# Performance work log

Measured on AMD Instinct MI355X. Metric: run time of the kernel, lower is better.

## Reference

```python
import jax, jax.numpy as jnp
from jax import lax
import numpy as np

B, CIN, H, W = 32, 256, 56, 56
BOTTLE, GROWTH = 128, 32
EPS = 1e-5
QMAX = 127.0  # 8-bit symmetric


def _fq(x, scale, qmax=QMAX):
    # fake-quantize with straight-through estimator
    q = jnp.clip(jnp.round(x / scale), -qmax - 1.0, qmax) * scale
    return x + lax.stop_gradient(q - x)


def fake_quant_act(x):
    # per-tensor symmetric 8-bit activation quantization (QuantAct)
    scale = lax.stop_gradient(jnp.max(jnp.abs(x)) / QMAX + 1e-8)
    return _fq(x, scale), scale


def quant_weight_pc(w):
    # per-output-channel symmetric 8-bit weight quantization, w: [O,I,kh,kw]
    scale = lax.stop_gradient(jnp.max(jnp.abs(w), axis=(1, 2, 3)) / QMAX + 1e-8)
    return _fq(w, scale[:, None, None, None]), scale


def conv2d(x, w, pad):
    return lax.conv_general_dilated(
        x, w, window_strides=(1, 1), padding=[(pad, pad), (pad, pad)],
        dimension_numbers=("NCHW", "OIHW", "NCHW"))


def setup_inputs() -> dict:
    key = jax.random.key(0)
    ks = jax.random.split(key, 12)
    return {
        "batch": jax.random.normal(ks[0], (B, CIN, H, W), jnp.float32),
        "input_scaling_factor": jnp.float32(0.05),
        "bn1_gamma": jax.random.uniform(ks[1], (CIN,), jnp.float32, 0.5, 1.5),
        "bn1_beta": jax.random.normal(ks[2], (CIN,), jnp.float32) * 0.1,
        "bn1_mean": jax.random.normal(ks[3], (CIN,), jnp.float32) * 0.1,
        "bn1_var": jax.random.uniform(ks[4], (CIN,), jnp.float32, 0.5, 1.5),
        "conv1_w": jax.random.normal(ks[5], (BOTTLE, CIN, 1, 1), jnp.float32) * 0.05,
        "bn2_gamma": jax.random.uniform(ks[6], (BOTTLE,), jnp.float32, 0.5, 1.5),
        "bn2_beta": jax.random.normal(ks[7], (BOTTLE,), jnp.float32) * 0.1,
        "bn2_mean": jax.random.normal(ks[8], (BOTTLE,), jnp.float32) * 0.1,
        "bn2_var": jax.random.uniform(ks[9], (BOTTLE,), jnp.float32, 0.5, 1.5),
        "conv2_w": jax.random.normal(ks[10], (GROWTH, BOTTLE, 3, 3), jnp.float32) * 0.05,
    }


def reference(batch, input_scaling_factor, bn1_gamma, bn1_beta, bn1_mean,
              bn1_var, conv1_w, bn2_gamma, bn2_beta, bn2_mean, bn2_var,
              conv2_w):
    s_in = input_scaling_factor
    # ---- QuantBn1: BN with fake-quantized folded weight/bias ----
    w1 = bn1_gamma * lax.rsqrt(bn1_var + EPS)            # [CIN]
    b1 = bn1_beta - bn1_mean * w1                        # [CIN]
    s_bn = lax.stop_gradient(jnp.max(jnp.abs(w1)) / QMAX + 1e-8)
    w1q = _fq(w1, s_bn)
    b1q = _fq(b1, s_in * s_bn, qmax=2.0 ** 31)           # bias quantized at s_in*s_w
    x = batch * w1q[None, :, None, None] + b1q[None, :, None, None]
    x = jax.nn.relu(x)                                   # act1
    x, s_a1 = fake_quant_act(x)                          # quant_act1
    # ---- QuantBnConv2d: fold bn2 into conv1 (1x1), per-channel weight quant ----
    t = bn2_gamma * lax.rsqrt(bn2_var + EPS)             # [BOTTLE]
    wf = conv1_w * t[:, None, None, None]
    bf = bn2_beta - bn2_mean * t
    wfq, s_w1 = quant_weight_pc(wf)                      # s_w1: [BOTTLE]
    bfq = _fq(bf, s_a1 * s_w1, qmax=2.0 ** 31)
    x = conv2d(x, wfq, pad=0) + bfq[None, :, None, None]
    x = jax.nn.relu(x)                                   # act2
    x, s_a2 = fake_quant_act(x)                          # quant_act2
    # ---- QuantConv2d: 3x3 growth conv, per-channel weight quant ----
    w2q, s_w2 = quant_weight_pc(conv2_w)
    x = conv2d(x, w2q, pad=1)                            # [B, GROWTH, H, W]
    # ---- concat + output requant ----
    cat = jnp.concatenate([batch, x], axis=1)            # [B, CIN+GROWTH, H, W]
    out, s_out = fake_quant_act(cat)                     # quant_act_output
    return out, s_out
```

## Files before the change

### kernel.cpp

```cpp
#include <hip/hip_runtime.h>

typedef __attribute__((ext_vector_type(8))) short bf16x8;
typedef __attribute__((ext_vector_type(4))) float f32x4;

constexpr int B_   = 32;
constexpr int CIN  = 256;
constexpr int HW   = 56 * 56;
constexpr int BOT  = 128;
constexpr int GRW  = 32;
constexpr int COUT = CIN + GRW;
constexpr int NBATCH = B_ * CIN * HW;
constexpr int NX2    = B_ * BOT * HW;
constexpr int NOUT   = B_ * COUT * HW;

constexpr int NSLOT = 32;
constexpr int SSTR  = 32;
constexpr int OFF_SLOT = 16;
constexpr int OFF_W1Q  = OFF_SLOT + 4 * NSLOT * SSTR;
constexpr int OFF_B1Q  = OFF_W1Q + 256;
constexpr int OFF_BFQ  = OFF_B1Q + 256;
constexpr int OFF_SC1  = OFF_BFQ + 128;
constexpr int OFF_SC2  = OFF_SC1 + 128;
constexpr int OFF_WQ1B = OFF_SC2 + 32;
constexpr int OFF_W2B  = OFF_WQ1B + 16384;
constexpr int OFF_END  = OFF_W2B + 18432;
constexpr size_t X1Q_BYTE = (size_t)OFF_END * 4;
constexpr size_t X2_BYTE  = X1Q_BYTE + (size_t)NBATCH;
constexpr size_t X2Q_BYTE = X1Q_BYTE;
constexpr size_t X3_BYTE  = X2_BYTE + (size_t)NX2 * 4;

__device__ __forceinline__ void slotAtomicMax(float* ws, int a, int s, float v) {
    atomicMax((unsigned*)ws + OFF_SLOT + a * NSLOT * SSTR + s * SSTR, __float_as_uint(v));
}
__device__ __forceinline__ float slotMax(const float* ws, int a) {
    float m = 0.0f;
    #pragma unroll
    for (int s = 0; s < NSLOT; s++)
        m = fmaxf(m, ws[OFF_SLOT + a * NSLOT * SSTR + s * SSTR]);
    return m;
}

__device__ __forceinline__ float blockReduceMax256(float v) {
    #pragma unroll
    for (int o = 32; o > 0; o >>= 1) v = fmaxf(v, __shfl_down(v, o, 64));
    __shared__ float sm[4];
    if ((threadIdx.x & 63) == 0) sm[threadIdx.x >> 6] = v;
    __syncthreads();
    return fmaxf(fmaxf(sm[0], sm[1]), fmaxf(sm[2], sm[3]));
}
__device__ __forceinline__ float waveReduceMax(float v) {
    #pragma unroll
    for (int o = 32; o > 0; o >>= 1) v = fmaxf(v, __shfl_down(v, o, 64));
    return v;
}
__device__ __forceinline__ float clamp8(float r)   { return fminf(fmaxf(r, -128.0f), 127.0f); }
__device__ __forceinline__ float clampBig(float r) { return fminf(fmaxf(r, -2147483648.0f), 2147483648.0f); }
__device__ __forceinline__ unsigned short bf16u(float f) { return (unsigned short)(__float_as_uint(f) >> 16); }

__device__ __forceinline__ bf16x8 b8_to_bf16(uint2 p) {
    bf16x8 r;
    #pragma unroll
    for (int j = 0; j < 4; j++) r[j]     = (short)bf16u((float)((p.x >> (j * 8)) & 255u));
    #pragma unroll
    for (int j = 0; j < 4; j++) r[4 + j] = (short)bf16u((float)((p.y >> (j * 8)) & 255u));
    return r;
}

__global__ void prep1_kernel(const float* __restrict__ g1, const float* __restrict__ b1p,
                             const float* __restrict__ m1, const float* __restrict__ v1,
                             const float* __restrict__ s_in_p, float* __restrict__ ws) {
    int c = threadIdx.x;
    unsigned* scal = (unsigned*)ws;
    for (int s = c; s < OFF_W1Q; s += 256) scal[s] = 0u;
    float s_in = *s_in_p;
    float r = 1.0f / sqrtf(v1[c] + 1e-5f);
    float w1 = __fmul_rn(g1[c], r);
    float b1 = __fsub_rn(b1p[c], __fmul_rn(m1[c], w1));
    float mx = blockReduceMax256(fabsf(w1));
    float s_bn = mx / 127.0f + 1e-8f;
    ws[OFF_W1Q + c] = __fmul_rn(clamp8(rintf(w1 / s_bn)), s_bn);
    float sb = __fmul_rn(s_in, s_bn);
    ws[OFF_B1Q + c] = __fmul_rn(clampBig(rintf(b1 / sb)), sb);
}

__global__ __launch_bounds__(256) void max1_kernel(const float4* __restrict__ batch4,
                                                   float* __restrict__ ws) {
    const float* w1q = ws + OFF_W1Q;
    const float* b1q = ws + OFF_B1Q;
    int n4 = NBATCH / 4;
    float mx1 = 0.0f, mxb = 0.0f;
    for (int i = blockIdx.x * blockDim.x + threadIdx.x; i < n4; i += gridDim.x * blockDim.x) {
        int c = (i / 784) & 255;
        float w = w1q[c], b = b1q[c];
        float4 v = batch4[i];
        float x0 = fmaxf(__fadd_rn(__fmul_rn(v.x, w), b), 0.0f);
        float x1 = fmaxf(__fadd_rn(__fmul_rn(v.y, w), b), 0.0f);
        float x2 = fmaxf(__fadd_rn(__fmul_rn(v.z, w), b), 0.0f);
        float x3 = fmaxf(__fadd_rn(__fmul_rn(v.w, w), b), 0.0f);
        mx1 = fmaxf(mx1, fmaxf(fmaxf(x0, x1), fmaxf(x2, x3)));
        mxb = fmaxf(mxb, fmaxf(fmaxf(fabsf(v.x), fabsf(v.y)), fmaxf(fabsf(v.z), fabsf(v.w))));
    }
    mx1 = blockReduceMax256(mx1);
    __syncthreads();
    mxb = blockReduceMax256(mxb);
    if (threadIdx.x == 0) {
        int s = blockIdx.x & (NSLOT - 1);
        slotAtomicMax(ws, 0, s, mx1);
        slotAtomicMax(ws, 1, s, mxb);
    }
}

__global__ __launch_bounds__(256) void quant1_kernel(const float4* __restrict__ batch4,
                                                     float* __restrict__ ws) {
    __shared__ unsigned ldsq[256 * 16];
    const float* w1q = ws + OFF_W1Q;
    const float* b1q = ws + OFF_B1Q;
    float s_a1 = slotMax(ws, 0) / 127.0f + 1e-8f;
    int b = blockIdx.x / 49, hw0 = (blockIdx.x % 49) * 64;
    int t = threadIdx.x;
    int f = t & 15, cb = t >> 4;
    #pragma unroll
    for (int j = 0; j < 16; j++) {
        int c = cb + j * 16;
        float w = w1q[c], bb = b1q[c];
        float4 v = batch4[(b * 256 + c) * 784 + (hw0 >> 2) + f];
        unsigned q0 = (unsigned)(int)clamp8(rintf(fmaxf(__fadd_rn(__fmul_rn(v.x, w), bb), 0.0f) / s_a1));
        unsigned q1 = (unsigned)(int)clamp8(rintf(fmaxf(__fadd_rn(__fmul_rn(v.y, w), bb), 0.0f) / s_a1));
        unsigned q2 = (unsigned)(int)clamp8(rintf(fmaxf(__fadd_rn(__fmul_rn(v.z, w), bb), 0.0f) / s_a1));
        unsigned q3 = (unsigned)(int)clamp8(rintf(fmaxf(__fadd_rn(__fmul_rn(v.w, w), bb), 0.0f) / s_a1));
        ldsq[c * 16 + f] = q0 | (q1 << 8) | (q2 << 16) | (q3 << 24);
    }
    __syncthreads();
    const unsigned char* l8 = (const unsigned char*)ldsq;
    uint4* outv = (uint4*)((char*)ws + X1Q_BYTE);
    int hwl = t >> 2, cq = (t & 3) * 16;
    #pragma unroll
    for (int k = 0; k < 4; k++) {
        int c0 = cq + k * 64;
        unsigned u[4] = {0u, 0u, 0u, 0u};
        #pragma unroll
        for (int i = 0; i < 16; i++) {
            unsigned by = l8[(c0 + i) * 64 + hwl];
            u[i >> 2] |= by << ((i & 3) * 8);
        }
        uint4 val; val.x = u[0]; val.y = u[1]; val.z = u[2]; val.w = u[3];
        outv[(((size_t)b * 3136 + hw0 + hwl) * 256 + c0) >> 4] = val;
    }
}

__global__ void prep2_kernel(const float* __restrict__ c1w,
                             const float* __restrict__ g2, const float* __restrict__ b2,
                             const float* __restrict__ m2, const float* __restrict__ v2,
                             const float* __restrict__ c2w, float* __restrict__ ws) {
    int bi = blockIdx.x;
    int t = threadIdx.x;
    unsigned short* wq1b = (unsigned short*)(ws + OFF_WQ1B);
    unsigned short* w2b  = (unsigned short*)(ws + OFF_W2B);
    if (bi < BOT) {
        int o = bi;
        float tt = __fmul_rn(g2[o], 1.0f / sqrtf(v2[o] + 1e-5f));
        float wf = __fmul_rn(c1w[o * CIN + t], tt);
        float mx = blockReduceMax256(fabsf(wf));
        float s_w1 = mx / 127.0f + 1e-8f;
        float m = clamp8(rintf(wf / s_w1));
        wq1b[o * CIN + t] = bf16u(m);
        if (t == 0) {
            float s_a1 = slotMax(ws, 0) / 127.0f + 1e-8f;
            ws[OFF_SC1 + o] = __fmul_rn(s_a1, s_w1);
            float bf = __fsub_rn(b2[o], __fmul_rn(m2[o], tt));
            float sb = __fmul_rn(s_a1, s_w1);
            ws[OFF_BFQ + o] = __fmul_rn(clampBig(rintf(bf / sb)), sb);
        }
    } else {
        int g = bi - BOT;
        float mx = 0.0f;
        for (int s = t; s < BOT * 9; s += 256) mx = fmaxf(mx, fabsf(c2w[g * BOT * 9 + s]));
        mx = blockReduceMax256(mx);
        float s_w2 = mx / 127.0f + 1e-8f;
        for (int s = t; s < BOT * 9; s += 256) {
            int c = s / 9, tap = s - c * 9;
            float m = clamp8(rintf(c2w[g * BOT * 9 + s] / s_w2));
            w2b[(tap * GRW + g) * BOT + c] = bf16u(m);
        }
        if (t == 0) ws[OFF_SC2 + g] = s_w2;
    }
}

__global__ __launch_bounds__(256) void conv1_kernel(float* __restrict__ ws) {
    __shared__ unsigned short lA[64 * 136];
    __shared__ unsigned short lW[128 * 136];
    __shared__ float wred[4];
    const unsigned char* x1q = (const unsigned char*)((char*)ws + X1Q_BYTE);
    const unsigned short* wq1b = (const unsigned short*)(ws + OFF_WQ1B);
    const float* sc1 = ws + OFF_SC1;
    const float* bfq = ws + OFF_BFQ;
    float* x2 = (float*)((char*)ws + X2_BYTE);
    int b = blockIdx.x / 49, hw0 = (blockIdx.x % 49) * 64;
    int t = threadIdx.x, lane = t & 63, wv = t >> 6;
    int quad = lane >> 4, l16 = lane & 15;
    int mhalf = wv & 1, nhalf = wv >> 1;
    f32x4 acc[2][4];
    #pragma unroll
    for (int i = 0; i < 2; i++)
        #pragma unroll
        for (int j = 0; j < 4; j++) acc[i][j] = (f32x4){0.f, 0.f, 0.f, 0.f};

    for (int kc = 0; kc < 256; kc += 128) {
        __syncthreads();
        {
            int cb = t & 7, hwi = t >> 3;
            #pragma unroll
            for (int r = 0; r < 2; r++) {
                int hw = hwi + r * 32;
                uint4 p = *(const uint4*)(x1q + ((size_t)b * 3136 + hw0 + hw) * 256 + kc + cb * 16);
                unsigned wd[4] = {p.x, p.y, p.z, p.w};
                bf16x8 t0, t1;
                #pragma unroll
                for (int j = 0; j < 8; j++)
                    t0[j] = (short)bf16u((float)((wd[j >> 2] >> ((j & 3) * 8)) & 255u));
                #pragma unroll
                for (int j = 0; j < 8; j++)
                    t1[j] = (short)bf16u((float)((wd[2 + (j >> 2)] >> ((j & 3) * 8)) & 255u));
                *(bf16x8*)&lA[hw * 136 + cb * 16] = t0;
                *(bf16x8*)&lA[hw * 136 + cb * 16 + 8] = t1;
            }
        }
        {
            int cb = t & 7, oi = t >> 3;
            #pragma unroll
            for (int r = 0; r < 4; r++) {
                int o = oi + r * 32;
                uint4 p0 = *(const uint4*)(wq1b + o * 256 + kc + cb * 16);
                uint4 p1 = *(const uint4*)(wq1b + o * 256 + kc + cb * 16 + 8);
                *(uint4*)&lW[o * 136 + cb * 16] = p0;
                *(uint4*)&lW[o * 136 + cb * 16 + 8] = p1;
            }
        }
        __syncthreads();
        #pragma unroll
        for (int ks = 0; ks < 4; ks++) {
            bf16x8 a0 = *(const bf16x8*)&lA[(mhalf * 32 + l16) * 136 + ks * 32 + quad * 8];
            bf16x8 a1 = *(const bf16x8*)&lA[(mhalf * 32 + 16 + l16) * 136 + ks * 32 + quad * 8];
            #pragma unroll
            for (int nt = 0; nt < 4; nt++) {
                bf16x8 bfr = *(const bf16x8*)&lW[(nhalf * 64 + nt * 16 + l16) * 136 + ks * 32 + quad * 8];
                acc[0][nt] = __builtin_amdgcn_mfma_f32_16x16x32_bf16(a0, bfr, acc[0][nt], 0, 0, 0);
                acc[1][nt] = __builtin_amdgcn_mfma_f32_16x16x32_bf16(a1, bfr, acc[1][nt], 0, 0, 0);
            }
        }
    }
    float mx = 0.0f;
    #pragma unroll
    for (int nt = 0; nt < 4; nt++) {
        int o = nhalf * 64 + nt * 16 + l16;
        float s = sc1[o], bb = bfq[o];
        #pragma unroll
        for (int mt = 0; mt < 2; mt++) {
            int hw = hw0 + mhalf * 32 + mt * 16 + quad * 4;
            float4 v;
            v.x = fmaxf(__fadd_rn(__fmul_rn(acc[mt][nt][0], s), bb), 0.0f);
            v.y = fmaxf(__fadd_rn(__fmul_rn(acc[mt][nt][1], s), bb), 0.0f);
            v.z = fmaxf(__fadd_rn(__fmul_rn(acc[mt][nt][2], s), bb), 0.0f);
            v.w = fmaxf(__fadd_rn(__fmul_rn(acc[mt][nt][3], s), bb), 0.0f);
            mx = fmaxf(mx, fmaxf(fmaxf(v.x, v.y), fmaxf(v.z, v.w)));
            *(float4*)&x2[(size_t)(b * BOT + o) * HW + hw] = v;
        }
    }
    mx = waveReduceMax(mx);
    if (lane == 0) wred[wv] = mx;
    __syncthreads();
    if (t == 0) {
        float m = fmaxf(fmaxf(wred[0], wred[1]), fmaxf(wred[2], wred[3]));
        slotAtomicMax(ws, 2, blockIdx.x & (NSLOT - 1), m);
    }
}

__global__ __launch_bounds__(256) void quant2_kernel(float* __restrict__ ws) {
    __shared__ unsigned ldsq[128 * 16];
    unsigned char* x2q = (unsigned char*)((char*)ws + X2Q_BYTE);
    int b = blockIdx.x / 58, hp = blockIdx.x % 58;
    int t = threadIdx.x;
    uint4* dst = (uint4*)(x2q + ((size_t)(b * 58 + hp) << 13));
    if (hp == 0 || hp == 57) {
        uint4 z; z.x = z.y = z.z = z.w = 0u;
        dst[t] = z; dst[t + 256] = z;
        return;
    }
    int h = hp - 1;
    float s_a2 = slotMax(ws, 2) / 127.0f + 1e-8f;
    float rinv = 1.0f / s_a2;
    const float4* x24 = (const float4*)((char*)ws + X2_BYTE);
    int f = t & 15, cb = t >> 4;
    #pragma unroll
    for (int j = 0; j < 8; j++) {
        int c = cb + j * 16;
        unsigned pk = 0u;
        if (f < 14) {
            float4 v = x24[((size_t)b * 128 + c) * 784 + h * 14 + f];
            unsigned q0 = (unsigned)(int)clamp8(rintf(v.x * rinv)) & 255u;
            unsigned q1 = (unsigned)(int)clamp8(rintf(v.y * rinv)) & 255u;
            unsigned q2 = (unsigned)(int)clamp8(rintf(v.z * rinv)) & 255u;
            unsigned q3 = (unsigned)(int)clamp8(rintf(v.w * rinv)) & 255u;
            pk = q0 | (q1 << 8) | (q2 << 16) | (q3 << 24);
        }
        ldsq[c * 16 + f] = pk;
    }
    __syncthreads();
    const unsigned char* l8 = (const unsigned char*)ldsq;
    #pragma unroll
    for (int k = 0; k < 2; k++) {
        int idx = t + k * 256;
        int wp = idx & 63, cblk = idx >> 6;
        int c0 = cblk * 16;
        unsigned u[4] = {0u, 0u, 0u, 0u};
        if (wp >= 1 && wp <= 56) {
            #pragma unroll
            for (int i = 0; i < 16; i++) {
                unsigned by = l8[(c0 + i) * 64 + (wp - 1)];
                u[i >> 2] |= by << ((i & 3) * 8);
            }
        }
        uint4 val; val.x = u[0]; val.y = u[1]; val.z = u[2]; val.w = u[3];
        dst[wp * 8 + cblk] = val;
    }
}

__global__ __launch_bounds__(256) void conv2_kernel(float* __restrict__ ws) {
    __shared__ unsigned short wt[9 * 32 * 40];
    __shared__ float wred[4];
    const unsigned char* x2q = (const unsigned char*)((char*)ws + X2Q_BYTE);
    const unsigned short* w2b = (const unsigned short*)(ws + OFF_W2B);
    const float* sc2 = ws + OFF_SC2;
    float* x3 = (float*)((char*)ws + X3_BYTE);
    int b = blockIdx.x / 28, hg = blockIdx.x % 28;
    int t = threadIdx.x, lane = t & 63, wv = t >> 6;
    int quad = lane >> 4, l16 = lane & 15;
    int h = hg * 2 + (wv >> 1);
    int wq = wv & 1;
    int w0 = wq * 24;
    float s_a2 = slotMax(ws, 2) / 127.0f + 1e-8f;

    const unsigned char* rowp[2][3];
    #pragma unroll
    for (int mt = 0; mt < 2; mt++) {
        int w = w0 + mt * 16 + l16;
        #pragma unroll
        for (int dh = 0; dh < 3; dh++)
            rowp[mt][dh] = x2q + (((size_t)(b * 58 + h + dh) << 6) + w) * 128 + quad * 8;
    }
    f32x4 acc[2][2];
    #pragma unroll
    for (int i = 0; i < 2; i++) { acc[i][0] = (f32x4){0.f,0.f,0.f,0.f}; acc[i][1] = (f32x4){0.f,0.f,0.f,0.f}; }

    for (int cs = 0; cs < 4; cs++) {
        __syncthreads();
        for (int s = t; s < 1152; s += 256) {
            int gi = s >> 2, q = s & 3;
            *(uint4*)&wt[gi * 40 + q * 8] = *(const uint4*)(w2b + gi * 128 + cs * 32 + q * 8);
        }
        __syncthreads();
        #pragma unroll
        for (int tap = 0; tap < 9; tap++) {
            int dh = tap / 3, dw = tap % 3;
            bf16x8 b0 = *(const bf16x8*)&wt[(tap * 32 + l16) * 40 + quad * 8];
            bf16x8 b1 = *(const bf16x8*)&wt[(tap * 32 + 16 + l16) * 40 + quad * 8];
            #pragma unroll
            for (int mt = 0; mt < 2; mt++) {
                uint2 p = *(const uint2*)(rowp[mt][dh] + dw * 128 + cs * 32);
                bf16x8 a = b8_to_bf16(p);
                acc[mt][0] = __builtin_amdgcn_mfma_f32_16x16x32_bf16(a, b0, acc[mt][0], 0, 0, 0);
                acc[mt][1] = __builtin_amdgcn_mfma_f32_16x16x32_bf16(a, b1, acc[mt][1], 0, 0, 0);
            }
        }
    }
    float mx = 0.0f;
    #pragma unroll
    for (int nt = 0; nt < 2; nt++) {
        int g = nt * 16 + l16;
        float s2 = __fmul_rn(s_a2, sc2[g]);
        #pragma unroll
        for (int mt = 0; mt < 2; mt++) {
            int wb = w0 + mt * 16 + quad * 4;
            if (wq == 0 || wb >= 32) {
                float4 v;
                v.x = __fmul_rn(acc[mt][nt][0], s2);
                v.y = __fmul_rn(acc[mt][nt][1], s2);
                v.z = __fmul_rn(acc[mt][nt][2], s2);
                v.w = __fmul_rn(acc[mt][nt][3], s2);
                mx = fmaxf(mx, fmaxf(fmaxf(fabsf(v.x), fabsf(v.y)), fmaxf(fabsf(v.z), fabsf(v.w))));
                *(float4*)&x3[(size_t)(b * GRW + g) * HW + h * 56 + wb] = v;
            }
        }
    }
    mx = waveReduceMax(mx);
    if (lane == 0) wred[wv] = mx;
    __syncthreads();
    if (t == 0) {
        float m = fmaxf(fmaxf(wred[0], wred[1]), fmaxf(wred[2], wred[3]));
        slotAtomicMax(ws, 3, blockIdx.x & (NSLOT - 1), m);
    }
}

__global__ __launch_bounds__(256) void outq_kernel(const float4* __restrict__ batch4,
                                                   const float* __restrict__ ws,
                                                   float* __restrict__ out) {
    const float4* x34 = (const float4*)((const char*)ws + X3_BYTE);
    float maxb = slotMax(ws, 1);
    float max3 = slotMax(ws, 3);
    float s_out = fmaxf(maxb, max3) / 127.0f + 1e-8f;
    float4* out4 = (float4*)out;
    int n4 = NOUT / 4;
    for (int i = blockIdx.x * blockDim.x + threadIdx.x; i < n4; i += gridDim.x * blockDim.x) {
        int chl = i / 784;
        int b = chl / COUT;
        int ch = chl - b * COUT;
        int hw4 = i - chl * 784;
        float4 v;
        if (ch < CIN) v = batch4[(b * CIN + ch) * 784 + hw4];
        else          v = x34[(b * GRW + (ch - CIN)) * 784 + hw4];
        float4 r;
        r.x = __fmul_rn(clamp8(rintf(v.x / s_out)), s_out);
        r.y = __fmul_rn(clamp8(rintf(v.y / s_out)), s_out);
        r.z = __fmul_rn(clamp8(rintf(v.z / s_out)), s_out);
        r.w = __fmul_rn(clamp8(rintf(v.w / s_out)), s_out);
        out4[i] = r;
    }
    if (blockIdx.x == 0 && threadIdx.x == 0) out[NOUT] = s_out;
}

extern "C" void kernel_launch(void* const* d_in, const int* in_sizes, int n_in,
                              void* d_out, int out_size, void* d_ws, size_t ws_size,
                              hipStream_t stream) {
    const float* batch = (const float*)d_in[0];
    const float* s_in  = (const float*)d_in[1];
    const float* g1    = (const float*)d_in[2];
    const float* b1    = (const float*)d_in[3];
    const float* m1    = (const float*)d_in[4];
    const float* v1    = (const float*)d_in[5];
    const float* c1w   = (const float*)d_in[6];
    const float* g2    = (const float*)d_in[7];
    const float* b2    = (const float*)d_in[8];
    const float* m2    = (const float*)d_in[9];
    const float* v2    = (const float*)d_in[10];
    const float* c2w   = (const float*)d_in[11];
    float* out = (float*)d_out;
    float* ws  = (float*)d_ws;

    hipLaunchKernelGGL(prep1_kernel, dim3(1), dim3(256), 0, stream, g1, b1, m1, v1, s_in, ws);
    hipLaunchKernelGGL(max1_kernel, dim3(2048), dim3(256), 0, stream, (const float4*)batch, ws);
    hipLaunchKernelGGL(quant1_kernel, dim3(32 * 49), dim3(256), 0, stream, (const float4*)batch, ws);
    hipLaunchKernelGGL(prep2_kernel, dim3(160), dim3(256), 0, stream, c1w, g2, b2, m2, v2, c2w, ws);
    hipLaunchKernelGGL(conv1_kernel, dim3(32 * 49), dim3(256), 0, stream, ws);
    hipLaunchKernelGGL(quant2_kernel, dim3(32 * 58), dim3(256), 0, stream, ws);
    hipLaunchKernelGGL(conv2_kernel, dim3(32 * 28), dim3(256), 0, stream, ws);
    hipLaunchKernelGGL(outq_kernel, dim3(4096), dim3(256), 0, stream, (const float4*)batch, ws, out);
}
```

Before: 342.0 us.

## Store quantized conv2 input as bf16, pad LDS transposes, restructure max1 indexing

quant2 now writes the padded conv2 input directly as bf16 values instead of int8 bytes. conv2 can then load bf16x8 operands straight from memory with no per-element byte-to-bf16 conversion, at the cost of doubling that buffer's traffic. The LDS transpose buffers in quant1 and quant2 get padded row strides to reduce bank conflicts. max1 now uses a fixed 512-block grid in which each thread walks one channel row, hoisting the per-element channel division and weight loads out of the loop.

```diff
diff --git a/kernel.cpp b/kernel.cpp
--- a/kernel.cpp
+++ b/kernel.cpp
@@ -26,8 +26,8 @@
 constexpr int OFF_END  = OFF_W2B + 18432;
 constexpr size_t X1Q_BYTE = (size_t)OFF_END * 4;
 constexpr size_t X2_BYTE  = X1Q_BYTE + (size_t)NBATCH;
-constexpr size_t X2Q_BYTE = X1Q_BYTE;
 constexpr size_t X3_BYTE  = X2_BYTE + (size_t)NX2 * 4;
+constexpr size_t X2B_BYTE = X3_BYTE + (size_t)(B_ * GRW * HW) * 4;
 
 __device__ __forceinline__ void slotAtomicMax(float* ws, int a, int s, float v) {
     atomicMax((unsigned*)ws + OFF_SLOT + a * NSLOT * SSTR + s * SSTR, __float_as_uint(v));
@@ -56,15 +56,6 @@
 __device__ __forceinline__ float clamp8(float r)   { return fminf(fmaxf(r, -128.0f), 127.0f); }
 __device__ __forceinline__ float clampBig(float r) { return fminf(fmaxf(r, -2147483648.0f), 2147483648.0f); }
 __device__ __forceinline__ unsigned short bf16u(float f) { return (unsigned short)(__float_as_uint(f) >> 16); }
-
-__device__ __forceinline__ bf16x8 b8_to_bf16(uint2 p) {
-    bf16x8 r;
-    #pragma unroll
-    for (int j = 0; j < 4; j++) r[j]     = (short)bf16u((float)((p.x >> (j * 8)) & 255u));
-    #pragma unroll
-    for (int j = 0; j < 4; j++) r[4 + j] = (short)bf16u((float)((p.y >> (j * 8)) & 255u));
-    return r;
-}
 
 __global__ void prep1_kernel(const float* __restrict__ g1, const float* __restrict__ b1p,
                              const float* __restrict__ m1, const float* __restrict__ v1,
@@ -87,12 +78,16 @@
                                                    float* __restrict__ ws) {
     const float* w1q = ws + OFF_W1Q;
     const float* b1q = ws + OFF_B1Q;
-    int n4 = NBATCH / 4;
+    int tid = blockIdx.x * 256 + threadIdx.x;
+    int row = tid >> 4;
+    int f   = tid & 15;
+    int c   = row & 255;
+    float w = w1q[c], b = b1q[c];
+    const float4* p = batch4 + (size_t)row * 784 + f;
     float mx1 = 0.0f, mxb = 0.0f;
-    for (int i = blockIdx.x * blockDim.x + threadIdx.x; i < n4; i += gridDim.x * blockDim.x) {
-        int c = (i / 784) & 255;
-        float w = w1q[c], b = b1q[c];
-        float4 v = batch4[i];
+    #pragma unroll 7
+    for (int k = 0; k < 49; k++) {
+        float4 v = p[k * 16];
         float x0 = fmaxf(__fadd_rn(__fmul_rn(v.x, w), b), 0.0f);
         float x1 = fmaxf(__fadd_rn(__fmul_rn(v.y, w), b), 0.0f);
         float x2 = fmaxf(__fadd_rn(__fmul_rn(v.z, w), b), 0.0f);
@@ -112,7 +107,7 @@
 
 __global__ __launch_bounds__(256) void quant1_kernel(const float4* __restrict__ batch4,
                                                      float* __restrict__ ws) {
-    __shared__ unsigned ldsq[256 * 16];
+    __shared__ unsigned ldsq[256 * 17];
     const float* w1q = ws + OFF_W1Q;
     const float* b1q = ws + OFF_B1Q;
     float s_a1 = slotMax(ws, 0) / 127.0f + 1e-8f;
@@ -128,7 +123,7 @@
         unsigned q1 = (unsigned)(int)clamp8(rintf(fmaxf(__fadd_rn(__fmul_rn(v.y, w), bb), 0.0f) / s_a1));
         unsigned q2 = (unsigned)(int)clamp8(rintf(fmaxf(__fadd_rn(__fmul_rn(v.z, w), bb), 0.0f) / s_a1));
         unsigned q3 = (unsigned)(int)clamp8(rintf(fmaxf(__fadd_rn(__fmul_rn(v.w, w), bb), 0.0f) / s_a1));
-        ldsq[c * 16 + f] = q0 | (q1 << 8) | (q2 << 16) | (q3 << 24);
+        ldsq[c * 17 + f] = q0 | (q1 << 8) | (q2 << 16) | (q3 << 24);
     }
     __syncthreads();
     const unsigned char* l8 = (const unsigned char*)ldsq;
@@ -140,7 +135,7 @@
         unsigned u[4] = {0u, 0u, 0u, 0u};
         #pragma unroll
         for (int i = 0; i < 16; i++) {
-            unsigned by = l8[(c0 + i) * 64 + hwl];
+            unsigned by = l8[(c0 + i) * 68 + hwl];
             u[i >> 2] |= by << ((i & 3) * 8);
         }
         uint4 val; val.x = u[0]; val.y = u[1]; val.z = u[2]; val.w = u[3];
@@ -276,59 +271,58 @@
 }
 
 __global__ __launch_bounds__(256) void quant2_kernel(float* __restrict__ ws) {
-    __shared__ unsigned ldsq[128 * 16];
-    unsigned char* x2q = (unsigned char*)((char*)ws + X2Q_BYTE);
+    __shared__ unsigned short lt[128 * 66];
+    unsigned short* x2b = (unsigned short*)((char*)ws + X2B_BYTE);
     int b = blockIdx.x / 58, hp = blockIdx.x % 58;
     int t = threadIdx.x;
-    uint4* dst = (uint4*)(x2q + ((size_t)(b * 58 + hp) << 13));
+    uint4* dst = (uint4*)(x2b + (size_t)(b * 58 + hp) * 8192);
     if (hp == 0 || hp == 57) {
         uint4 z; z.x = z.y = z.z = z.w = 0u;
-        dst[t] = z; dst[t + 256] = z;
+        #pragma unroll
+        for (int k = 0; k < 4; k++) dst[t + k * 256] = z;
         return;
     }
     int h = hp - 1;
     float s_a2 = slotMax(ws, 2) / 127.0f + 1e-8f;
     float rinv = 1.0f / s_a2;
     const float4* x24 = (const float4*)((char*)ws + X2_BYTE);
+    unsigned* ltw = (unsigned*)lt;
     int f = t & 15, cb = t >> 4;
-    #pragma unroll
-    for (int j = 0; j < 8; j++) {
-        int c = cb + j * 16;
-        unsigned pk = 0u;
-        if (f < 14) {
+    if (f < 14) {
+        #pragma unroll
+        for (int j = 0; j < 8; j++) {
+            int c = cb + j * 16;
             float4 v = x24[((size_t)b * 128 + c) * 784 + h * 14 + f];
-            unsigned q0 = (unsigned)(int)clamp8(rintf(v.x * rinv)) & 255u;
-            unsigned q1 = (unsigned)(int)clamp8(rintf(v.y * rinv)) & 255u;
-            unsigned q2 = (unsigned)(int)clamp8(rintf(v.z * rinv)) & 255u;
-            unsigned q3 = (unsigned)(int)clamp8(rintf(v.w * rinv)) & 255u;
-            pk = q0 | (q1 << 8) | (q2 << 16) | (q3 << 24);
-        }
-        ldsq[c * 16 + f] = pk;
-    }
-    __syncthreads();
-    const unsigned char* l8 = (const unsigned char*)ldsq;
-    #pragma unroll
-    for (int k = 0; k < 2; k++) {
+            unsigned q0 = bf16u(clamp8(rintf(v.x * rinv)));
+            unsigned q1 = bf16u(clamp8(rintf(v.y * rinv)));
+            unsigned q2 = bf16u(clamp8(rintf(v.z * rinv)));
+            unsigned q3 = bf16u(clamp8(rintf(v.w * rinv)));
+            ltw[c * 33 + f * 2]     = q0 | (q1 << 16);
+            ltw[c * 33 + f * 2 + 1] = q2 | (q3 << 16);
+        }
+    }
+    __syncthreads();
+    #pragma unroll
+    for (int k = 0; k < 4; k++) {
         int idx = t + k * 256;
-        int wp = idx & 63, cblk = idx >> 6;
-        int c0 = cblk * 16;
+        int cblk = idx & 15, wp = idx >> 4;
         unsigned u[4] = {0u, 0u, 0u, 0u};
         if (wp >= 1 && wp <= 56) {
             #pragma unroll
-            for (int i = 0; i < 16; i++) {
-                unsigned by = l8[(c0 + i) * 64 + (wp - 1)];
-                u[i >> 2] |= by << ((i & 3) * 8);
+            for (int i = 0; i < 8; i++) {
+                unsigned s = lt[(cblk * 8 + i) * 66 + (wp - 1)];
+                u[i >> 1] |= s << ((i & 1) * 16);
             }
         }
         uint4 val; val.x = u[0]; val.y = u[1]; val.z = u[2]; val.w = u[3];
-        dst[wp * 8 + cblk] = val;
+        dst[wp * 16 + cblk] = val;
     }
 }
 
 __global__ __launch_bounds__(256) void conv2_kernel(float* __restrict__ ws) {
     __shared__ unsigned short wt[9 * 32 * 40];
     __shared__ float wred[4];
-    const unsigned char* x2q = (const unsigned char*)((char*)ws + X2Q_BYTE);
+    const unsigned short* x2b = (const unsigned short*)((char*)ws + X2B_BYTE);
     const unsigned short* w2b = (const unsigned short*)(ws + OFF_W2B);
     const float* sc2 = ws + OFF_SC2;
     float* x3 = (float*)((char*)ws + X3_BYTE);
@@ -340,13 +334,13 @@
     int w0 = wq * 24;
     float s_a2 = slotMax(ws, 2) / 127.0f + 1e-8f;
 
-    const unsigned char* rowp[2][3];
+    const unsigned short* rowp[2][3];
     #pragma unroll
     for (int mt = 0; mt < 2; mt++) {
         int w = w0 + mt * 16 + l16;
         #pragma unroll
         for (int dh = 0; dh < 3; dh++)
-            rowp[mt][dh] = x2q + (((size_t)(b * 58 + h + dh) << 6) + w) * 128 + quad * 8;
+            rowp[mt][dh] = x2b + ((size_t)(b * 58 + h + dh) * 64 + w) * 128 + quad * 8;
     }
     f32x4 acc[2][2];
     #pragma unroll
@@ -366,8 +360,7 @@
             bf16x8 b1 = *(const bf16x8*)&wt[(tap * 32 + 16 + l16) * 40 + quad * 8];
             #pragma unroll
             for (int mt = 0; mt < 2; mt++) {
-                uint2 p = *(const uint2*)(rowp[mt][dh] + dw * 128 + cs * 32);
-                bf16x8 a = b8_to_bf16(p);
+                bf16x8 a = *(const bf16x8*)(rowp[mt][dh] + dw * 128 + cs * 32);
                 acc[mt][0] = __builtin_amdgcn_mfma_f32_16x16x32_bf16(a, b0, acc[mt][0], 0, 0, 0);
                 acc[mt][1] = __builtin_amdgcn_mfma_f32_16x16x32_bf16(a, b1, acc[mt][1], 0, 0, 0);
             }
@@ -447,7 +440,7 @@
     float* ws  = (float*)d_ws;
 
     hipLaunchKernelGGL(prep1_kernel, dim3(1), dim3(256), 0, stream, g1, b1, m1, v1, s_in, ws);
-    hipLaunchKernelGGL(max1_kernel, dim3(2048), dim3(256), 0, stream, (const float4*)batch, ws);
+    hipLaunchKernelGGL(max1_kernel, dim3(512), dim3(256), 0, stream, (const float4*)batch, ws);
     hipLaunchKernelGGL(quant1_kernel, dim3(32 * 49), dim3(256), 0, stream, (const float4*)batch, ws);
     hipLaunchKernelGGL(prep2_kernel, dim3(160), dim3(256), 0, stream, c1w, g2, b2, m2, v2, c2w, ws);
     hipLaunchKernelGGL(conv1_kernel, dim3(32 * 49), dim3(256), 0, stream, ws);
```

Result: no change. 345.3 us (+1.0%).
